# Kernel optimization log

Hardware: AMD Instinct MI355X
Metric: run time of the kernel (lower is better)

The kernel has to match this reference:

```python
import jax, jax.numpy as jnp
import numpy as np

T, B, H, L = 64, 128, 256, 2  # steps/stack_size, batch, hidden, layers


def setup_inputs() -> dict:
    key = jax.random.key(0)
    ks = jax.random.split(key, 6)
    s = 1.0 / np.sqrt(H)
    x = jax.random.normal(ks[0], (T, B, H), dtype=jnp.float32)
    ops = jax.random.randint(ks[1], (T, B), 0, 2, dtype=jnp.int32)  # push=1, hold=0
    W_ih = jax.random.uniform(ks[2], (L, 4 * H, H), jnp.float32, -s, s)
    W_hh = jax.random.uniform(ks[3], (L, 4 * H, H), jnp.float32, -s, s)
    b_ih = jax.random.uniform(ks[4], (L, 4 * H), jnp.float32, -s, s)
    b_hh = jax.random.uniform(ks[5], (L, 4 * H), jnp.float32, -s, s)
    return {"x": x, "ops": ops, "W_ih": W_ih, "W_hh": W_hh, "b_ih": b_ih, "b_hh": b_hh}


def reference(x, ops, W_ih, W_hh, b_ih, b_hh):
    T_, B_, H_ = x.shape
    L_ = W_ih.shape[0]
    bidx = jnp.arange(B_)

    def cell(xt, h_prev, c_prev):
        # multi-layer LSTM cell; layer l>0 takes layer l-1 hidden as input (dropout=0)
        inp = xt
        hs, cs = [], []
        for l in range(L_):
            gates = inp @ W_ih[l].T + b_ih[l] + h_prev[..., l] @ W_hh[l].T + b_hh[l]
            i, f, g, o = jnp.split(gates, 4, axis=-1)
            c = jax.nn.sigmoid(f) * c_prev[..., l] + jax.nn.sigmoid(i) * jnp.tanh(g)
            h = jax.nn.sigmoid(o) * jnp.tanh(c)
            hs.append(h)
            cs.append(c)
            inp = h
        return jnp.stack(hs, axis=-1), jnp.stack(cs, axis=-1)  # (B, H, L)

    def step(carry, xt_op):
        hstack, cstack, pos = carry  # stacks: (T+1, B, H, L), pos: (B,)
        xt, opt = xt_op
        h_prev = hstack[pos, bidx]  # gather top-of-stack, (B, H, L)
        c_prev = cstack[pos, bidx]
        nh, nc = cell(xt, h_prev, c_prev)
        # hold_or_push writes at pos+1 for every batch element, then pos += op
        hstack = hstack.at[pos + 1, bidx].set(nh)
        cstack = cstack.at[pos + 1, bidx].set(nc)
        pos = pos + opt
        return (hstack, cstack, pos), nh[..., -1]  # last-layer hidden output

    hs0 = jnp.zeros((T_ + 1, B_, H_, L_), dtype=x.dtype)
    cs0 = jnp.zeros((T_ + 1, B_, H_, L_), dtype=x.dtype)
    pos0 = jnp.zeros((B_,), dtype=jnp.int32)
    _, outs = jax.lax.scan(step, (hs0, cs0, pos0), (x, ops))
    return outs  # (T, B, H)
```

## Files before the change

kernel.cpp:

```cpp
#include <hip/hip_runtime.h>
#include <hip/hip_fp16.h>
#include <cstddef>

#define TT 64
#define BB 128
#define HH 256
#define G4 1024
#define BLK 256
#define NBG 32
#define NHG 16

#define OFF_XG     0u
#define OFF_WTIH0  8388608u
#define OFF_HX0    8650752u
#define OFF_HX1    8716288u

__device__ __forceinline__ float sigf(float x) { return 1.0f / (1.0f + expf(-x)); }

typedef _Float16 h2v __attribute__((ext_vector_type(2)));

__device__ __forceinline__ float dot2acc(unsigned w, unsigned h, float acc) {
#if __has_builtin(__builtin_amdgcn_fdot2)
  return __builtin_amdgcn_fdot2(__builtin_bit_cast(h2v, w),
                                __builtin_bit_cast(h2v, h), acc, false);
#else
  __half2 wv = *(__half2*)&w, hv = *(__half2*)&h;
  float2 wf = __half22float2(wv), hf = __half22float2(hv);
  return fmaf(wf.x, hf.x, fmaf(wf.y, hf.y, acc));
#endif
}

__device__ __forceinline__ unsigned packh2(float e, float o) {
  return (unsigned)__half_as_ushort(__float2half(e)) |
         ((unsigned)__half_as_ushort(__float2half(o)) << 16);
}

__device__ __forceinline__ int hsw(int b, int k2) {
  return b * 144 + k2 + ((k2 >> 5) << 2);
}

__global__ void transpose1(const float* __restrict__ W_ih, float* __restrict__ ws) {
  __shared__ float tile[32][33];
  float* dst = ws + OFF_WTIH0;
  const int g0 = blockIdx.x * 32, k0 = blockIdx.y * 32;
  const int tx = threadIdx.x, ty = threadIdx.y;
#pragma unroll
  for (int i = 0; i < 32; i += 8)
    tile[ty + i][tx] = W_ih[(size_t)(g0 + ty + i) * HH + k0 + tx];
  __syncthreads();
#pragma unroll
  for (int i = 0; i < 32; i += 8)
    dst[(size_t)(k0 + ty + i) * G4 + g0 + tx] = tile[tx][ty + i];
}

__global__ void xg_kernel(const float* __restrict__ x,
                          const float* __restrict__ b_ih,
                          float* __restrict__ ws) {
  const float* __restrict__ WTih0 = ws + OFF_WTIH0;
  float* __restrict__ Xg = ws + OFF_XG;
  const int r0 = blockIdx.x * 16;
  const int g = blockIdx.y * 256 + threadIdx.x;
  __shared__ float xs[16][HH];
  for (int i = threadIdx.x; i < 16 * HH; i += 256)
    xs[i >> 8][i & 255] = x[(size_t)(r0 + (i >> 8)) * HH + (i & 255)];
  __syncthreads();
  float acc[16];
  const float bias = b_ih[g];
#pragma unroll
  for (int r = 0; r < 16; ++r) acc[r] = bias;
  for (int k = 0; k < HH; ++k) {
    const float w = WTih0[(size_t)k * G4 + g];
#pragma unroll
    for (int r = 0; r < 16; ++r) acc[r] = fmaf(xs[r][k], w, acc[r]);
  }
  const int hg = (g >> 4) & 15;
  const int lc = ((g >> 8) << 4) | (g & 15);
#pragma unroll
  for (int r = 0; r < 16; ++r) {
    const int rr = r0 + r;
    const int t = rr >> 7, b = rr & 127;
    Xg[(((size_t)t * NHG + hg) * 128 + b) * 64 + lc] = acc[r];
  }
}

__global__ void __launch_bounds__(BLK, 2)
seq9(const float* __restrict__ W_ih,
     const float* __restrict__ W_hh,
     const float* __restrict__ b_ih,
     const float* __restrict__ b_hh,
     const int* __restrict__ ops,
     float* __restrict__ ws,
     float* __restrict__ out) {
  const int bg = blockIdx.x & 31;
  const int hg = blockIdx.x >> 5;
  const int tid = threadIdx.x;
  const int kq = tid & 7;
  const int c2 = tid >> 3;

  __shared__ __align__(16) float XgL[TT * 256];
  __shared__ __align__(16) unsigned hp0[4 * 144];
  __shared__ __align__(16) unsigned hp1[4 * 144];
  __shared__ __align__(16) unsigned h0c[4 * 144];
  __shared__ float gatA[256];
  __shared__ float gatB[256];
  __shared__ int opsA[TT * 4];

  unsigned wr0[32], wr1[32], wr2[32];
  {
    const float* s0 = W_hh;
    const float* s1 = W_ih + (size_t)G4 * HH;
    const float* s2 = W_hh + (size_t)G4 * HH;
#pragma unroll
    for (int j = 0; j < 2; ++j) {
      const int lc = c2 * 2 + j;
      const int g = ((lc >> 4) << 8) + hg * 16 + (lc & 15);
      const float* p0 = s0 + (size_t)g * HH + kq * 32;
      const float* p1 = s1 + (size_t)g * HH + kq * 32;
      const float* p2 = s2 + (size_t)g * HH + kq * 32;
#pragma unroll
      for (int i = 0; i < 16; ++i) {
        wr0[j * 16 + i] = packh2(p0[2 * i], p0[2 * i + 1]);
        wr1[j * 16 + i] = packh2(p1[2 * i], p1[2 * i + 1]);
        wr2[j * 16 + i] = packh2(p2[2 * i], p2[2 * i + 1]);
      }
    }
  }
  float bias0r[2], bias1r[2];
#pragma unroll
  for (int j = 0; j < 2; ++j) {
    const int lc = c2 * 2 + j;
    const int g = ((lc >> 4) << 8) + hg * 16 + (lc & 15);
    bias0r[j] = b_hh[g];
    bias1r[j] = b_ih[G4 + g] + b_hh[G4 + g];
  }
  for (int i = tid; i < TT * 64; i += BLK) {
    const int t = i >> 6, r = i & 63;
    ((float4*)XgL)[i] = *(const float4*)(
        ws + OFF_XG + (((size_t)t * NHG + hg) * 128 + bg * 4) * 64 + r * 4);
  }
  for (int i = tid; i < TT * 4; i += BLK)
    opsA[i] = ops[(i >> 2) * BB + bg * 4 + (i & 3)];
  for (int i = tid; i < 4 * 144; i += BLK) { hp0[i] = 0u; hp1[i] = 0u; }

  unsigned long long* __restrict__ Hx0 = (unsigned long long*)(ws + OFF_HX0);
  unsigned long long* __restrict__ Hx1 = (unsigned long long*)(ws + OFF_HX1);
  float cp0 = 0.f, cp1 = 0.f;
  float a0r[4][2] = {{0.f, 0.f}, {0.f, 0.f}, {0.f, 0.f}, {0.f, 0.f}};
  float a1q[4][2] = {{0.f, 0.f}, {0.f, 0.f}, {0.f, 0.f}, {0.f, 0.f}};
  __syncthreads();

  for (int t = 0; t < TT; ++t) {
    const int par = t & 1;

#pragma unroll
    for (int b = 0; b < 4; ++b) {
      if (t > 0 && opsA[(t - 1) * 4 + b]) {
        const unsigned* hb = &hp0[b * 144 + kq * 16 + ((kq >> 1) << 2)];
        const uint4 x0 = *(const uint4*)(hb + 0);
        const uint4 x1 = *(const uint4*)(hb + 4);
        const uint4 x2 = *(const uint4*)(hb + 8);
        const uint4 x3 = *(const uint4*)(hb + 12);
        const unsigned hh[16] = {x0.x, x0.y, x0.z, x0.w, x1.x, x1.y, x1.z, x1.w,
                                 x2.x, x2.y, x2.z, x2.w, x3.x, x3.y, x3.z, x3.w};
        float s0 = 0.f, s1 = 0.f;
#pragma unroll
        for (int i = 0; i < 16; ++i) {
          s0 = dot2acc(wr0[i], hh[i], s0);
          s1 = dot2acc(wr0[16 + i], hh[i], s1);
        }
#pragma unroll
        for (int m = 1; m <= 4; m <<= 1) {
          s0 += __shfl_xor(s0, m, 64);
          s1 += __shfl_xor(s1, m, 64);
        }
        a0r[b][0] = s0;
        a0r[b][1] = s1;
      }
    }
    if (kq == 0) {
#pragma unroll
      for (int b = 0; b < 4; ++b)
        *(float2*)&gatA[b * 64 + c2 * 2] =
            make_float2(a0r[b][0] + bias0r[0], a0r[b][1] + bias0r[1]);
    }
    __syncthreads();

    if (tid < 64) {
      const int b = tid >> 4, r = tid & 15;
      const float* xg = &XgL[t * 256 + b * 64];
      const float* gt = &gatA[b * 64];
      const float ig = gt[r] + xg[r],           fg = gt[16 + r] + xg[16 + r];
      const float gg = gt[32 + r] + xg[32 + r], og = gt[48 + r] + xg[48 + r];
      const float c = sigf(fg) * cp0 + sigf(ig) * tanhf(gg);
      const float h = sigf(og) * tanhf(c);
      if (opsA[t * 4 + b]) cp0 = c;
      const float ho = __shfl_xor(h, 1, 64);
      if (!(r & 1)) {
        const unsigned long long v =
            (unsigned long long)(unsigned)(t + 1) |
            ((unsigned long long)packh2(h, ho) << 32);
        __hip_atomic_store(
            Hx0 + ((size_t)par * NBG + bg) * 512 + b * 128 + hg * 8 + (r >> 1),
            v, __ATOMIC_RELAXED, __HIP_MEMORY_SCOPE_AGENT);
      }
    }

    {
      const unsigned long long* s0 = Hx0 + ((size_t)par * NBG + bg) * 512;
      const unsigned long long* s1 = Hx1 + ((size_t)(par ^ 1) * NBG + bg) * 512;
      const unsigned tagA = (unsigned)(t + 1);
      const unsigned tagB = (unsigned)t;
      const int idx1 = tid + 256;
      const int b0 = tid >> 7, k20 = tid & 127;
      const int b1 = idx1 >> 7, k21 = idx1 & 127;
      const bool need1a = (t > 0) && (opsA[(t - 1) * 4 + b0] != 0);
      const bool need1b = (t > 0) && (opsA[(t - 1) * 4 + b1] != 0);
      unsigned long long v0 = 0, v1 = 0, w0 = 0, w1 = 0;
      bool d0 = false, d1 = false, e0 = !need1a, e1 = !need1b;
      int spins = 0;
      for (;;) {
        if (!d0) v0 = __hip_atomic_load(s0 + tid, __ATOMIC_RELAXED,
                                        __HIP_MEMORY_SCOPE_AGENT);
        if (!d1) v1 = __hip_atomic_load(s0 + idx1, __ATOMIC_RELAXED,
                                        __HIP_MEMORY_SCOPE_AGENT);
        if (!e0) w0 = __hip_atomic_load(s1 + tid, __ATOMIC_RELAXED,
                                        __HIP_MEMORY_SCOPE_AGENT);
        if (!e1) w1 = __hip_atomic_load(s1 + idx1, __ATOMIC_RELAXED,
                                        __HIP_MEMORY_SCOPE_AGENT);
        d0 = d0 || ((unsigned)v0 == tagA);
        d1 = d1 || ((unsigned)v1 == tagA);
        e0 = e0 || ((unsigned)w0 == tagB);
        e1 = e1 || ((unsigned)w1 == tagB);
        if (d0 && d1 && e0 && e1) break;
        if (++spins > (1 << 18)) break;
        if (spins > 2) __builtin_amdgcn_s_sleep(1);
      }
      const unsigned p0 = (unsigned)(v0 >> 32), p1 = (unsigned)(v1 >> 32);
      const int sw0 = hsw(b0, k20), sw1 = hsw(b1, k21);
      h0c[sw0] = p0;
      h0c[sw1] = p1;
      if (opsA[t * 4 + b0]) hp0[sw0] = p0;
      if (opsA[t * 4 + b1]) hp0[sw1] = p1;
      if (need1a) hp1[sw0] = (unsigned)(w0 >> 32);
      if (need1b) hp1[sw1] = (unsigned)(w1 >> 32);
    }
    __syncthreads();

    float fr[4][2];
#pragma unroll
    for (int b = 0; b < 4; ++b) {
      const unsigned* cb = &h0c[b * 144 + kq * 16 + ((kq >> 1) << 2)];
      const uint4 c0 = *(const uint4*)(cb + 0);
      const uint4 c1 = *(const uint4*)(cb + 4);
      const uint4 c2v = *(const uint4*)(cb + 8);
      const uint4 c3 = *(const uint4*)(cb + 12);
      const unsigned hc[16] = {c0.x, c0.y, c0.z, c0.w, c1.x, c1.y, c1.z, c1.w,
                               c2v.x, c2v.y, c2v.z, c2v.w, c3.x, c3.y, c3.z, c3.w};
      float s0 = 0.f, s1 = 0.f;
#pragma unroll
      for (int i = 0; i < 16; ++i) {
        s0 = dot2acc(wr1[i], hc[i], s0);
        s1 = dot2acc(wr1[16 + i], hc[i], s1);
      }
      if (t > 0 && opsA[(t - 1) * 4 + b]) {
        const unsigned* qb = &hp1[b * 144 + kq * 16 + ((kq >> 1) << 2)];
        const uint4 q0 = *(const uint4*)(qb + 0);
        const uint4 q1 = *(const uint4*)(qb + 4);
        const uint4 q2 = *(const uint4*)(qb + 8);
        const uint4 q3 = *(const uint4*)(qb + 12);
        const unsigned hq[16] = {q0.x, q0.y, q0.z, q0.w, q1.x, q1.y, q1.z, q1.w,
                                 q2.x, q2.y, q2.z, q2.w, q3.x, q3.y, q3.z, q3.w};
        float t0 = 0.f, t1 = 0.f;
#pragma unroll
        for (int i = 0; i < 16; ++i) {
          t0 = dot2acc(wr2[i], hq[i], t0);
          t1 = dot2acc(wr2[16 + i], hq[i], t1);
        }
#pragma unroll
        for (int m = 1; m <= 4; m <<= 1) {
          t0 += __shfl_xor(t0, m, 64);
          t1 += __shfl_xor(t1, m, 64);
        }
        a1q[b][0] = t0;
        a1q[b][1] = t1;
      }
#pragma unroll
      for (int m = 1; m <= 4; m <<= 1) {
        s0 += __shfl_xor(s0, m, 64);
        s1 += __shfl_xor(s1, m, 64);
      }
      fr[b][0] = s0;
      fr[b][1] = s1;
    }
    if (kq == 0) {
#pragma unroll
      for (int b = 0; b < 4; ++b)
        *(float2*)&gatB[b * 64 + c2 * 2] =
            make_float2(fr[b][0] + a1q[b][0] + bias1r[0],
                        fr[b][1] + a1q[b][1] + bias1r[1]);
    }
    __syncthreads();

    if (tid < 64) {
      const int b = tid >> 4, r = tid & 15;
      const float* gt = &gatB[b * 64];
      const float ig = gt[r],      fg = gt[16 + r];
      const float gg = gt[32 + r], og = gt[48 + r];
      const float c = sigf(fg) * cp1 + sigf(ig) * tanhf(gg);
      const float h = sigf(og) * tanhf(c);
      const int op = opsA[t * 4 + b];
      if (op) cp1 = c;
      out[((size_t)t * BB + bg * 4 + b) * HH + hg * 16 + r] = h;
      const float ho = __shfl_xor(h, 1, 64);
      if (op && !(r & 1)) {
        const unsigned long long v =
            (unsigned long long)(unsigned)(t + 1) |
            ((unsigned long long)packh2(h, ho) << 32);
        __hip_atomic_store(
            Hx1 + ((size_t)par * NBG + bg) * 512 + b * 128 + hg * 8 + (r >> 1),
            v, __ATOMIC_RELAXED, __HIP_MEMORY_SCOPE_AGENT);
      }
    }
  }
}

extern "C" void kernel_launch(void* const* d_in, const int* in_sizes, int n_in,
                              void* d_out, int out_size, void* d_ws, size_t ws_size,
                              hipStream_t stream) {
  const float* x    = (const float*)d_in[0];
  const int*   ops  = (const int*)d_in[1];
  const float* W_ih = (const float*)d_in[2];
  const float* W_hh = (const float*)d_in[3];
  const float* b_ih = (const float*)d_in[4];
  const float* b_hh = (const float*)d_in[5];
  float* out = (float*)d_out;
  float* ws  = (float*)d_ws;

  transpose1<<<dim3(32, 8), dim3(32, 8), 0, stream>>>(W_ih, ws);
  xg_kernel<<<dim3(512, 4), 256, 0, stream>>>(x, b_ih, ws);
  seq9<<<512, BLK, 0, stream>>>(W_ih, W_hh, b_ih, b_hh, ops, ws, out);
}
```

Before: 523.9 us.

## Split layers into separate pipelined block roles and fuse input projection

Replaces the three-kernel pipeline with one persistent kernel whose blocks take one of two roles: layer-0 blocks and layer-1 blocks, each handling 8 batch rows per block. Layer 0 now computes the x·W_ih projection in-kernel with double-buffered x loads, which removes the separate transpose and precompute kernels and their workspace traffic. Layer-1 blocks consume layer-0 hidden states through per-timestep tagged global buffers, so the two layers can run in a wavefront pipeline instead of serially within a block. The cost is more register pressure (64 fp32 weights per thread in layer 0), larger global handoff buffers, and cross-block spin waiting.

New measurement: 467.1 us. -10.8%, faster.

```diff
diff --git a/kernel.cpp b/kernel.cpp
--- a/kernel.cpp
+++ b/kernel.cpp
@@ -7,13 +7,8 @@
 #define HH 256
 #define G4 1024
 #define BLK 256
-#define NBG 32
+#define NBG 16
 #define NHG 16
-
-#define OFF_XG     0u
-#define OFF_WTIH0  8388608u
-#define OFF_HX0    8650752u
-#define OFF_HX1    8716288u
 
 __device__ __forceinline__ float sigf(float x) { return 1.0f / (1.0f + expf(-x)); }
 
@@ -35,290 +30,333 @@
          ((unsigned)__half_as_ushort(__float2half(o)) << 16);
 }
 
-__device__ __forceinline__ int hsw(int b, int k2) {
+__device__ __forceinline__ int hsw8(int b, int k2) {
   return b * 144 + k2 + ((k2 >> 5) << 2);
 }
 
-__global__ void transpose1(const float* __restrict__ W_ih, float* __restrict__ ws) {
-  __shared__ float tile[32][33];
-  float* dst = ws + OFF_WTIH0;
-  const int g0 = blockIdx.x * 32, k0 = blockIdx.y * 32;
-  const int tx = threadIdx.x, ty = threadIdx.y;
-#pragma unroll
-  for (int i = 0; i < 32; i += 8)
-    tile[ty + i][tx] = W_ih[(size_t)(g0 + ty + i) * HH + k0 + tx];
-  __syncthreads();
-#pragma unroll
-  for (int i = 0; i < 32; i += 8)
-    dst[(size_t)(k0 + ty + i) * G4 + g0 + tx] = tile[tx][ty + i];
-}
-
-__global__ void xg_kernel(const float* __restrict__ x,
-                          const float* __restrict__ b_ih,
-                          float* __restrict__ ws) {
-  const float* __restrict__ WTih0 = ws + OFF_WTIH0;
-  float* __restrict__ Xg = ws + OFF_XG;
-  const int r0 = blockIdx.x * 16;
-  const int g = blockIdx.y * 256 + threadIdx.x;
-  __shared__ float xs[16][HH];
-  for (int i = threadIdx.x; i < 16 * HH; i += 256)
-    xs[i >> 8][i & 255] = x[(size_t)(r0 + (i >> 8)) * HH + (i & 255)];
-  __syncthreads();
-  float acc[16];
-  const float bias = b_ih[g];
-#pragma unroll
-  for (int r = 0; r < 16; ++r) acc[r] = bias;
-  for (int k = 0; k < HH; ++k) {
-    const float w = WTih0[(size_t)k * G4 + g];
-#pragma unroll
-    for (int r = 0; r < 16; ++r) acc[r] = fmaf(xs[r][k], w, acc[r]);
-  }
-  const int hg = (g >> 4) & 15;
-  const int lc = ((g >> 8) << 4) | (g & 15);
-#pragma unroll
-  for (int r = 0; r < 16; ++r) {
-    const int rr = r0 + r;
-    const int t = rr >> 7, b = rr & 127;
-    Xg[(((size_t)t * NHG + hg) * 128 + b) * 64 + lc] = acc[r];
-  }
-}
-
 __global__ void __launch_bounds__(BLK, 2)
-seq9(const float* __restrict__ W_ih,
-     const float* __restrict__ W_hh,
-     const float* __restrict__ b_ih,
-     const float* __restrict__ b_hh,
-     const int* __restrict__ ops,
-     float* __restrict__ ws,
-     float* __restrict__ out) {
-  const int bg = blockIdx.x & 31;
-  const int hg = blockIdx.x >> 5;
+seq10(const float* __restrict__ x,
+      const int* __restrict__ ops,
+      const float* __restrict__ W_ih,
+      const float* __restrict__ W_hh,
+      const float* __restrict__ b_ih,
+      const float* __restrict__ b_hh,
+      float* __restrict__ ws,
+      float* __restrict__ out) {
+  const int role = blockIdx.x >> 8;
+  const int bh = blockIdx.x & 255;
+  const int bg = bh & 15;
+  const int hg = bh >> 4;
   const int tid = threadIdx.x;
   const int kq = tid & 7;
   const int c2 = tid >> 3;
 
-  __shared__ __align__(16) float XgL[TT * 256];
-  __shared__ __align__(16) unsigned hp0[4 * 144];
-  __shared__ __align__(16) unsigned hp1[4 * 144];
-  __shared__ __align__(16) unsigned h0c[4 * 144];
-  __shared__ float gatA[256];
-  __shared__ float gatB[256];
-  __shared__ int opsA[TT * 4];
-
-  unsigned wr0[32], wr1[32], wr2[32];
-  {
-    const float* s0 = W_hh;
-    const float* s1 = W_ih + (size_t)G4 * HH;
-    const float* s2 = W_hh + (size_t)G4 * HH;
+  __shared__ __align__(16) float smem[6272];
+  __shared__ int opsA[TT * 8];
+
+  unsigned long long* __restrict__ Hx0 = (unsigned long long*)ws;
+  unsigned long long* __restrict__ Hx1 = Hx0 + (size_t)TT * NBG * 1024;
+
+  for (int i = tid; i < TT * 8; i += BLK)
+    opsA[i] = ops[(i >> 3) * BB + bg * 8 + (i & 7)];
+
+  const int pb = tid >> 5;
+  const int pk2 = (tid & 31) * 4;
+
+  if (role == 0) {
+    float* xbufs = smem;
+    unsigned* hp0 = (unsigned*)(smem + 4608);
+    float* gatA = smem + 5760;
+
+    unsigned wr0[32];
+    float wx0[64];
+    float bias0r[2];
 #pragma unroll
     for (int j = 0; j < 2; ++j) {
       const int lc = c2 * 2 + j;
       const int g = ((lc >> 4) << 8) + hg * 16 + (lc & 15);
-      const float* p0 = s0 + (size_t)g * HH + kq * 32;
-      const float* p1 = s1 + (size_t)g * HH + kq * 32;
-      const float* p2 = s2 + (size_t)g * HH + kq * 32;
+      const float* ph = W_hh + (size_t)g * HH + kq * 32;
+      const float* pw = W_ih + (size_t)g * HH + kq * 32;
+#pragma unroll
+      for (int i = 0; i < 16; ++i)
+        wr0[j * 16 + i] = packh2(ph[2 * i], ph[2 * i + 1]);
+#pragma unroll
+      for (int i = 0; i < 32; ++i) wx0[j * 32 + i] = pw[i];
+      bias0r[j] = b_ih[g] + b_hh[g];
+    }
+    for (int i = tid; i < 8 * 144; i += BLK) hp0[i] = 0u;
+    {
+      const float4* xsrc = (const float4*)(x + (size_t)bg * 8 * HH);
+#pragma unroll
+      for (int i2 = 0; i2 < 2; ++i2) {
+        const int f4 = tid + i2 * 256;
+        const float4 v = xsrc[f4];
+        const int b = f4 >> 6, k4 = f4 & 63;
+        *(float4*)&xbufs[b * 288 + (k4 >> 3) * 36 + (k4 & 7) * 4] = v;
+      }
+    }
+    __syncthreads();
+
+    float xf[8][2];
+#pragma unroll
+    for (int b = 0; b < 8; ++b) {
+      const float* xb = &xbufs[b * 288 + kq * 36];
+      float s0 = 0.f, s1 = 0.f;
+#pragma unroll
+      for (int k = 0; k < 32; ++k) {
+        s0 = fmaf(wx0[k], xb[k], s0);
+        s1 = fmaf(wx0[32 + k], xb[k], s1);
+      }
+#pragma unroll
+      for (int m = 1; m <= 4; m <<= 1) {
+        s0 += __shfl_xor(s0, m, 64);
+        s1 += __shfl_xor(s1, m, 64);
+      }
+      xf[b][0] = s0; xf[b][1] = s1;
+    }
+    float a0r[8][2] = {};
+    float cp0 = 0.f;
+
+    for (int t = 0; t < TT; ++t) {
+      if (t > 0 && opsA[(t - 1) * 8 + pb]) {
+        const unsigned long long* sp = Hx0 + ((size_t)(t - 1) * NBG + bg) * 1024;
+        const unsigned tag = (unsigned)t;
+        unsigned long long v[4];
+        bool d[4] = {false, false, false, false};
+        int spins = 0;
+        for (;;) {
+#pragma unroll
+          for (int i = 0; i < 4; ++i)
+            if (!d[i]) v[i] = __hip_atomic_load(sp + tid * 4 + i, __ATOMIC_RELAXED,
+                                                __HIP_MEMORY_SCOPE_AGENT);
+          bool all = true;
+#pragma unroll
+          for (int i = 0; i < 4; ++i) { d[i] = d[i] || ((unsigned)v[i] == tag); all &= d[i]; }
+          if (all) break;
+          if (++spins > (1 << 18)) break;
+          if (spins > 2) __builtin_amdgcn_s_sleep(1);
+        }
+        *(uint4*)&hp0[hsw8(pb, pk2)] =
+            make_uint4((unsigned)(v[0] >> 32), (unsigned)(v[1] >> 32),
+                       (unsigned)(v[2] >> 32), (unsigned)(v[3] >> 32));
+      }
+      __syncthreads();
+
+#pragma unroll
+      for (int b = 0; b < 8; ++b) {
+        if (t > 0 && opsA[(t - 1) * 8 + b]) {
+          const unsigned* hb = &hp0[b * 144 + kq * 16 + ((kq >> 1) << 2)];
+          const uint4 x0 = *(const uint4*)(hb + 0);
+          const uint4 x1 = *(const uint4*)(hb + 4);
+          const uint4 x2 = *(const uint4*)(hb + 8);
+          const uint4 x3 = *(const uint4*)(hb + 12);
+          const unsigned hh[16] = {x0.x, x0.y, x0.z, x0.w, x1.x, x1.y, x1.z, x1.w,
+                                   x2.x, x2.y, x2.z, x2.w, x3.x, x3.y, x3.z, x3.w};
+          float s0 = 0.f, s1 = 0.f;
+#pragma unroll
+          for (int i = 0; i < 16; ++i) {
+            s0 = dot2acc(wr0[i], hh[i], s0);
+            s1 = dot2acc(wr0[16 + i], hh[i], s1);
+          }
+#pragma unroll
+          for (int m = 1; m <= 4; m <<= 1) {
+            s0 += __shfl_xor(s0, m, 64);
+            s1 += __shfl_xor(s1, m, 64);
+          }
+          a0r[b][0] = s0; a0r[b][1] = s1;
+        }
+      }
+      if (kq == 0) {
+#pragma unroll
+        for (int b = 0; b < 8; ++b)
+          *(float2*)&gatA[b * 64 + c2 * 2] =
+              make_float2(xf[b][0] + a0r[b][0] + bias0r[0],
+                          xf[b][1] + a0r[b][1] + bias0r[1]);
+      }
+      __syncthreads();
+
+      if (tid < 128) {
+        const int b = tid >> 4, r = tid & 15;
+        const float* gt = &gatA[b * 64];
+        const float ig = gt[r], fg = gt[16 + r], gg = gt[32 + r], og = gt[48 + r];
+        const float c = sigf(fg) * cp0 + sigf(ig) * tanhf(gg);
+        const float h = sigf(og) * tanhf(c);
+        if (opsA[t * 8 + b]) cp0 = c;
+        const float ho = __shfl_xor(h, 1, 64);
+        if (!(r & 1)) {
+          const unsigned long long vv =
+              (unsigned long long)(unsigned)(t + 1) |
+              ((unsigned long long)packh2(h, ho) << 32);
+          __hip_atomic_store(
+              Hx0 + ((size_t)t * NBG + bg) * 1024 + b * 128 + hg * 8 + (r >> 1),
+              vv, __ATOMIC_RELAXED, __HIP_MEMORY_SCOPE_AGENT);
+        }
+      }
+      if (t < TT - 1) {
+        float* xd = &xbufs[((t + 1) & 1) * 2304];
+        const float4* xsrc = (const float4*)(x + ((size_t)(t + 1) * BB + bg * 8) * HH);
+#pragma unroll
+        for (int i2 = 0; i2 < 2; ++i2) {
+          const int f4 = tid + i2 * 256;
+          const float4 v = xsrc[f4];
+          const int b = f4 >> 6, k4 = f4 & 63;
+          *(float4*)&xd[b * 288 + (k4 >> 3) * 36 + (k4 & 7) * 4] = v;
+        }
+        __syncthreads();
+#pragma unroll
+        for (int b = 0; b < 8; ++b) {
+          const float* xb = &xd[b * 288 + kq * 36];
+          float s0 = 0.f, s1 = 0.f;
+#pragma unroll
+          for (int k = 0; k < 32; ++k) {
+            s0 = fmaf(wx0[k], xb[k], s0);
+            s1 = fmaf(wx0[32 + k], xb[k], s1);
+          }
+#pragma unroll
+          for (int m = 1; m <= 4; m <<= 1) {
+            s0 += __shfl_xor(s0, m, 64);
+            s1 += __shfl_xor(s1, m, 64);
+          }
+          xf[b][0] = s0; xf[b][1] = s1;
+        }
+      }
+    }
+  } else {
+    unsigned* h0c = (unsigned*)smem;
+    unsigned* hp1 = (unsigned*)(smem + 1152);
+    float* gatB = smem + 2304;
+
+    unsigned wr1[32], wr2[32];
+    float bias1r[2];
+#pragma unroll
+    for (int j = 0; j < 2; ++j) {
+      const int lc = c2 * 2 + j;
+      const int g = ((lc >> 4) << 8) + hg * 16 + (lc & 15);
+      const float* p1 = W_ih + (size_t)G4 * HH + (size_t)g * HH + kq * 32;
+      const float* p2 = W_hh + (size_t)G4 * HH + (size_t)g * HH + kq * 32;
 #pragma unroll
       for (int i = 0; i < 16; ++i) {
-        wr0[j * 16 + i] = packh2(p0[2 * i], p0[2 * i + 1]);
         wr1[j * 16 + i] = packh2(p1[2 * i], p1[2 * i + 1]);
         wr2[j * 16 + i] = packh2(p2[2 * i], p2[2 * i + 1]);
       }
-    }
-  }
-  float bias0r[2], bias1r[2];
-#pragma unroll
-  for (int j = 0; j < 2; ++j) {
-    const int lc = c2 * 2 + j;
-    const int g = ((lc >> 4) << 8) + hg * 16 + (lc & 15);
-    bias0r[j] = b_hh[g];
-    bias1r[j] = b_ih[G4 + g] + b_hh[G4 + g];
-  }
-  for (int i = tid; i < TT * 64; i += BLK) {
-    const int t = i >> 6, r = i & 63;
-    ((float4*)XgL)[i] = *(const float4*)(
-        ws + OFF_XG + (((size_t)t * NHG + hg) * 128 + bg * 4) * 64 + r * 4);
-  }
-  for (int i = tid; i < TT * 4; i += BLK)
-    opsA[i] = ops[(i >> 2) * BB + bg * 4 + (i & 3)];
-  for (int i = tid; i < 4 * 144; i += BLK) { hp0[i] = 0u; hp1[i] = 0u; }
-
-  unsigned long long* __restrict__ Hx0 = (unsigned long long*)(ws + OFF_HX0);
-  unsigned long long* __restrict__ Hx1 = (unsigned long long*)(ws + OFF_HX1);
-  float cp0 = 0.f, cp1 = 0.f;
-  float a0r[4][2] = {{0.f, 0.f}, {0.f, 0.f}, {0.f, 0.f}, {0.f, 0.f}};
-  float a1q[4][2] = {{0.f, 0.f}, {0.f, 0.f}, {0.f, 0.f}, {0.f, 0.f}};
-  __syncthreads();
-
-  for (int t = 0; t < TT; ++t) {
-    const int par = t & 1;
-
-#pragma unroll
-    for (int b = 0; b < 4; ++b) {
-      if (t > 0 && opsA[(t - 1) * 4 + b]) {
-        const unsigned* hb = &hp0[b * 144 + kq * 16 + ((kq >> 1) << 2)];
-        const uint4 x0 = *(const uint4*)(hb + 0);
-        const uint4 x1 = *(const uint4*)(hb + 4);
-        const uint4 x2 = *(const uint4*)(hb + 8);
-        const uint4 x3 = *(const uint4*)(hb + 12);
-        const unsigned hh[16] = {x0.x, x0.y, x0.z, x0.w, x1.x, x1.y, x1.z, x1.w,
-                                 x2.x, x2.y, x2.z, x2.w, x3.x, x3.y, x3.z, x3.w};
+      bias1r[j] = b_ih[G4 + g] + b_hh[G4 + g];
+    }
+    for (int i = tid; i < 8 * 144; i += BLK) hp1[i] = 0u;
+    float a1q[8][2] = {};
+    float cp1 = 0.f;
+    __syncthreads();
+
+    for (int t = 0; t < TT; ++t) {
+      {
+        const unsigned long long* sp0 = Hx0 + ((size_t)t * NBG + bg) * 1024;
+        const unsigned long long* sp1 =
+            Hx1 + ((size_t)(t > 0 ? t - 1 : 0) * NBG + bg) * 1024;
+        const unsigned tagA = (unsigned)(t + 1), tagB = (unsigned)t;
+        const bool need1 = (t > 0) && (opsA[(t - 1) * 8 + pb] != 0);
+        unsigned long long v[4], w[4];
+        bool dv[4] = {false, false, false, false};
+        bool dw[4] = {!need1, !need1, !need1, !need1};
+        int spins = 0;
+        for (;;) {
+#pragma unroll
+          for (int i = 0; i < 4; ++i) {
+            if (!dv[i]) v[i] = __hip_atomic_load(sp0 + tid * 4 + i, __ATOMIC_RELAXED,
+                                                 __HIP_MEMORY_SCOPE_AGENT);
+            if (!dw[i]) w[i] = __hip_atomic_load(sp1 + tid * 4 + i, __ATOMIC_RELAXED,
+                                                 __HIP_MEMORY_SCOPE_AGENT);
+          }
+          bool all = true;
+#pragma unroll
+          for (int i = 0; i < 4; ++i) {
+            dv[i] = dv[i] || ((unsigned)v[i] == tagA);
+            dw[i] = dw[i] || ((unsigned)w[i] == tagB);
+            all = all && dv[i] && dw[i];
+          }
+          if (all) break;
+          if (++spins > (1 << 18)) break;
+          if (spins > 2) __builtin_amdgcn_s_sleep(1);
+        }
+        *(uint4*)&h0c[hsw8(pb, pk2)] =
+            make_uint4((unsigned)(v[0] >> 32), (unsigned)(v[1] >> 32),
+                       (unsigned)(v[2] >> 32), (unsigned)(v[3] >> 32));
+        if (need1)
+          *(uint4*)&hp1[hsw8(pb, pk2)] =
+              make_uint4((unsigned)(w[0] >> 32), (unsigned)(w[1] >> 32),
+                         (unsigned)(w[2] >> 32), (unsigned)(w[3] >> 32));
+      }
+      __syncthreads();
+
+      float fr[8][2];
+#pragma unroll
+      for (int b = 0; b < 8; ++b) {
+        const unsigned* cb = &h0c[b * 144 + kq * 16 + ((kq >> 1) << 2)];
+        const uint4 c0 = *(const uint4*)(cb + 0);
+        const uint4 c1 = *(const uint4*)(cb + 4);
+        const uint4 c2v = *(const uint4*)(cb + 8);
+        const uint4 c3 = *(const uint4*)(cb + 12);
+        const unsigned hc[16] = {c0.x, c0.y, c0.z, c0.w, c1.x, c1.y, c1.z, c1.w,
+                                 c2v.x, c2v.y, c2v.z, c2v.w, c3.x, c3.y, c3.z, c3.w};
         float s0 = 0.f, s1 = 0.f;
 #pragma unroll
         for (int i = 0; i < 16; ++i) {
-          s0 = dot2acc(wr0[i], hh[i], s0);
-          s1 = dot2acc(wr0[16 + i], hh[i], s1);
+          s0 = dot2acc(wr1[i], hc[i], s0);
+          s1 = dot2acc(wr1[16 + i], hc[i], s1);
+        }
+        if (t > 0 && opsA[(t - 1) * 8 + b]) {
+          const unsigned* qb = &hp1[b * 144 + kq * 16 + ((kq >> 1) << 2)];
+          const uint4 q0 = *(const uint4*)(qb + 0);
+          const uint4 q1 = *(const uint4*)(qb + 4);
+          const uint4 q2 = *(const uint4*)(qb + 8);
+          const uint4 q3 = *(const uint4*)(qb + 12);
+          const unsigned hq[16] = {q0.x, q0.y, q0.z, q0.w, q1.x, q1.y, q1.z, q1.w,
+                                   q2.x, q2.y, q2.z, q2.w, q3.x, q3.y, q3.z, q3.w};
+          float t0 = 0.f, t1 = 0.f;
+#pragma unroll
+          for (int i = 0; i < 16; ++i) {
+            t0 = dot2acc(wr2[i], hq[i], t0);
+            t1 = dot2acc(wr2[16 + i], hq[i], t1);
+          }
+#pragma unroll
+          for (int m = 1; m <= 4; m <<= 1) {
+            t0 += __shfl_xor(t0, m, 64);
+            t1 += __shfl_xor(t1, m, 64);
+          }
+          a1q[b][0] = t0; a1q[b][1] = t1;
         }
 #pragma unroll
         for (int m = 1; m <= 4; m <<= 1) {
           s0 += __shfl_xor(s0, m, 64);
           s1 += __shfl_xor(s1, m, 64);
         }
-        a0r[b][0] = s0;
-        a0r[b][1] = s1;
-      }
-    }
-    if (kq == 0) {
-#pragma unroll
-      for (int b = 0; b < 4; ++b)
-        *(float2*)&gatA[b * 64 + c2 * 2] =
-            make_float2(a0r[b][0] + bias0r[0], a0r[b][1] + bias0r[1]);
-    }
-    __syncthreads();
-
-    if (tid < 64) {
-      const int b = tid >> 4, r = tid & 15;
-      const float* xg = &XgL[t * 256 + b * 64];
-      const float* gt = &gatA[b * 64];
-      const float ig = gt[r] + xg[r],           fg = gt[16 + r] + xg[16 + r];
-      const float gg = gt[32 + r] + xg[32 + r], og = gt[48 + r] + xg[48 + r];
-      const float c = sigf(fg) * cp0 + sigf(ig) * tanhf(gg);
-      const float h = sigf(og) * tanhf(c);
-      if (opsA[t * 4 + b]) cp0 = c;
-      const float ho = __shfl_xor(h, 1, 64);
-      if (!(r & 1)) {
-        const unsigned long long v =
-            (unsigned long long)(unsigned)(t + 1) |
-            ((unsigned long long)packh2(h, ho) << 32);
-        __hip_atomic_store(
-            Hx0 + ((size_t)par * NBG + bg) * 512 + b * 128 + hg * 8 + (r >> 1),
-            v, __ATOMIC_RELAXED, __HIP_MEMORY_SCOPE_AGENT);
-      }
-    }
-
-    {
-      const unsigned long long* s0 = Hx0 + ((size_t)par * NBG + bg) * 512;
-      const unsigned long long* s1 = Hx1 + ((size_t)(par ^ 1) * NBG + bg) * 512;
-      const unsigned tagA = (unsigned)(t + 1);
-      const unsigned tagB = (unsigned)t;
-      const int idx1 = tid + 256;
-      const int b0 = tid >> 7, k20 = tid & 127;
-      const int b1 = idx1 >> 7, k21 = idx1 & 127;
-      const bool need1a = (t > 0) && (opsA[(t - 1) * 4 + b0] != 0);
-      const bool need1b = (t > 0) && (opsA[(t - 1) * 4 + b1] != 0);
-      unsigned long long v0 = 0, v1 = 0, w0 = 0, w1 = 0;
-      bool d0 = false, d1 = false, e0 = !need1a, e1 = !need1b;
-      int spins = 0;
-      for (;;) {
-        if (!d0) v0 = __hip_atomic_load(s0 + tid, __ATOMIC_RELAXED,
-                                        __HIP_MEMORY_SCOPE_AGENT);
-        if (!d1) v1 = __hip_atomic_load(s0 + idx1, __ATOMIC_RELAXED,
-                                        __HIP_MEMORY_SCOPE_AGENT);
-        if (!e0) w0 = __hip_atomic_load(s1 + tid, __ATOMIC_RELAXED,
-                                        __HIP_MEMORY_SCOPE_AGENT);
-        if (!e1) w1 = __hip_atomic_load(s1 + idx1, __ATOMIC_RELAXED,
-                                        __HIP_MEMORY_SCOPE_AGENT);
-        d0 = d0 || ((unsigned)v0 == tagA);
-        d1 = d1 || ((unsigned)v1 == tagA);
-        e0 = e0 || ((unsigned)w0 == tagB);
-        e1 = e1 || ((unsigned)w1 == tagB);
-        if (d0 && d1 && e0 && e1) break;
-        if (++spins > (1 << 18)) break;
-        if (spins > 2) __builtin_amdgcn_s_sleep(1);
-      }
-      const unsigned p0 = (unsigned)(v0 >> 32), p1 = (unsigned)(v1 >> 32);
-      const int sw0 = hsw(b0, k20), sw1 = hsw(b1, k21);
-      h0c[sw0] = p0;
-      h0c[sw1] = p1;
-      if (opsA[t * 4 + b0]) hp0[sw0] = p0;
-      if (opsA[t * 4 + b1]) hp0[sw1] = p1;
-      if (need1a) hp1[sw0] = (unsigned)(w0 >> 32);
-      if (need1b) hp1[sw1] = (unsigned)(w1 >> 32);
-    }
-    __syncthreads();
-
-    float fr[4][2];
-#pragma unroll
-    for (int b = 0; b < 4; ++b) {
-      const unsigned* cb = &h0c[b * 144 + kq * 16 + ((kq >> 1) << 2)];
-      const uint4 c0 = *(const uint4*)(cb + 0);
-      const uint4 c1 = *(const uint4*)(cb + 4);
-      const uint4 c2v = *(const uint4*)(cb + 8);
-      const uint4 c3 = *(const uint4*)(cb + 12);
-      const unsigned hc[16] = {c0.x, c0.y, c0.z, c0.w, c1.x, c1.y, c1.z, c1.w,
-                               c2v.x, c2v.y, c2v.z, c2v.w, c3.x, c3.y, c3.z, c3.w};
-      float s0 = 0.f, s1 = 0.f;
-#pragma unroll
-      for (int i = 0; i < 16; ++i) {
-        s0 = dot2acc(wr1[i], hc[i], s0);
-        s1 = dot2acc(wr1[16 + i], hc[i], s1);
-      }
-      if (t > 0 && opsA[(t - 1) * 4 + b]) {
-        const unsigned* qb = &hp1[b * 144 + kq * 16 + ((kq >> 1) << 2)];
-        const uint4 q0 = *(const uint4*)(qb + 0);
-        const uint4 q1 = *(const uint4*)(qb + 4);
-        const uint4 q2 = *(const uint4*)(qb + 8);
-        const uint4 q3 = *(const uint4*)(qb + 12);
-        const unsigned hq[16] = {q0.x, q0.y, q0.z, q0.w, q1.x, q1.y, q1.z, q1.w,
-                                 q2.x, q2.y, q2.z, q2.w, q3.x, q3.y, q3.z, q3.w};
-        float t0 = 0.f, t1 = 0.f;
-#pragma unroll
-        for (int i = 0; i < 16; ++i) {
-          t0 = dot2acc(wr2[i], hq[i], t0);
-          t1 = dot2acc(wr2[16 + i], hq[i], t1);
-        }
-#pragma unroll
-        for (int m = 1; m <= 4; m <<= 1) {
-          t0 += __shfl_xor(t0, m, 64);
-          t1 += __shfl_xor(t1, m, 64);
-        }
-        a1q[b][0] = t0;
-        a1q[b][1] = t1;
-      }
-#pragma unroll
-      for (int m = 1; m <= 4; m <<= 1) {
-        s0 += __shfl_xor(s0, m, 64);
-        s1 += __shfl_xor(s1, m, 64);
-      }
-      fr[b][0] = s0;
-      fr[b][1] = s1;
-    }
-    if (kq == 0) {
-#pragma unroll
-      for (int b = 0; b < 4; ++b)
-        *(float2*)&gatB[b * 64 + c2 * 2] =
-            make_float2(fr[b][0] + a1q[b][0] + bias1r[0],
-                        fr[b][1] + a1q[b][1] + bias1r[1]);
-    }
-    __syncthreads();
-
-    if (tid < 64) {
-      const int b = tid >> 4, r = tid & 15;
-      const float* gt = &gatB[b * 64];
-      const float ig = gt[r],      fg = gt[16 + r];
-      const float gg = gt[32 + r], og = gt[48 + r];
-      const float c = sigf(fg) * cp1 + sigf(ig) * tanhf(gg);
-      const float h = sigf(og) * tanhf(c);
-      const int op = opsA[t * 4 + b];
-      if (op) cp1 = c;
-      out[((size_t)t * BB + bg * 4 + b) * HH + hg * 16 + r] = h;
-      const float ho = __shfl_xor(h, 1, 64);
-      if (op && !(r & 1)) {
-        const unsigned long long v =
-            (unsigned long long)(unsigned)(t + 1) |
-            ((unsigned long long)packh2(h, ho) << 32);
-        __hip_atomic_store(
-            Hx1 + ((size_t)par * NBG + bg) * 512 + b * 128 + hg * 8 + (r >> 1),
-            v, __ATOMIC_RELAXED, __HIP_MEMORY_SCOPE_AGENT);
+        fr[b][0] = s0; fr[b][1] = s1;
+      }
+      if (kq == 0) {
+#pragma unroll
+        for (int b = 0; b < 8; ++b)
+          *(float2*)&gatB[b * 64 + c2 * 2] =
+              make_float2(fr[b][0] + a1q[b][0] + bias1r[0],
+                          fr[b][1] + a1q[b][1] + bias1r[1]);
+      }
+      __syncthreads();
+
+      if (tid < 128) {
+        const int b = tid >> 4, r = tid & 15;
+        const float* gt = &gatB[b * 64];
+        const float ig = gt[r], fg = gt[16 + r], gg = gt[32 + r], og = gt[48 + r];
+        const float c = sigf(fg) * cp1 + sigf(ig) * tanhf(gg);
+        const float h = sigf(og) * tanhf(c);
+        const int op = opsA[t * 8 + b];
+        if (op) cp1 = c;
+        out[((size_t)t * BB + bg * 8 + b) * HH + hg * 16 + r] = h;
+        const float ho = __shfl_xor(h, 1, 64);
+        if (op && !(r & 1)) {
+          const unsigned long long vv =
+              (unsigned long long)(unsigned)(t + 1) |
+              ((unsigned long long)packh2(h, ho) << 32);
+          __hip_atomic_store(
+              Hx1 + ((size_t)t * NBG + bg) * 1024 + b * 128 + hg * 8 + (r >> 1),
+              vv, __ATOMIC_RELAXED, __HIP_MEMORY_SCOPE_AGENT);
+        }
       }
     }
   }
@@ -336,7 +374,5 @@
   float* out = (float*)d_out;
   float* ws  = (float*)d_ws;
 
-  transpose1<<<dim3(32, 8), dim3(32, 8), 0, stream>>>(W_ih, ws);
-  xg_kernel<<<dim3(512, 4), 256, 0, stream>>>(x, b_ih, ws);
-  seq9<<<512, BLK, 0, stream>>>(W_ih, W_hh, b_ih, b_hh, ops, ws, out);
-}
+  seq10<<<512, BLK, 0, stream>>>(x, ops, W_ih, W_hh, b_ih, b_hh, ws, out);
+}
```

## Fuse layer-0 input projection into the sequential LSTM kernel prologue

Applied to the files above, without the earlier changes.

Removes the separate weight-transpose and input-projection kernels. Each block of the persistent recurrent kernel now computes its own slice of the x·W_ih0 gate preactivations, using fp32 weights held in registers and shuffle reductions, and writes them straight into shared memory. This saves two kernel launches and the global round trip of the 8M-float Xg buffer. In exchange the prologue runs serially inside the recurrent kernel, keeps 64 extra registers live for a while, and each block reads x for its batch rows across all 64 steps.

Result: slower. 870.7 us (+66.2%).

```diff
diff --git a/kernel.cpp b/kernel.cpp
--- a/kernel.cpp
+++ b/kernel.cpp
@@ -8,12 +8,9 @@
 #define G4 1024
 #define BLK 256
 #define NBG 32
-#define NHG 16
-
-#define OFF_XG     0u
-#define OFF_WTIH0  8388608u
-#define OFF_HX0    8650752u
-#define OFF_HX1    8716288u
+
+#define OFF_HX0 0u
+#define OFF_HX1 65536u
 
 __device__ __forceinline__ float sigf(float x) { return 1.0f / (1.0f + expf(-x)); }
 
@@ -39,58 +36,15 @@
   return b * 144 + k2 + ((k2 >> 5) << 2);
 }
 
-__global__ void transpose1(const float* __restrict__ W_ih, float* __restrict__ ws) {
-  __shared__ float tile[32][33];
-  float* dst = ws + OFF_WTIH0;
-  const int g0 = blockIdx.x * 32, k0 = blockIdx.y * 32;
-  const int tx = threadIdx.x, ty = threadIdx.y;
-#pragma unroll
-  for (int i = 0; i < 32; i += 8)
-    tile[ty + i][tx] = W_ih[(size_t)(g0 + ty + i) * HH + k0 + tx];
-  __syncthreads();
-#pragma unroll
-  for (int i = 0; i < 32; i += 8)
-    dst[(size_t)(k0 + ty + i) * G4 + g0 + tx] = tile[tx][ty + i];
-}
-
-__global__ void xg_kernel(const float* __restrict__ x,
-                          const float* __restrict__ b_ih,
-                          float* __restrict__ ws) {
-  const float* __restrict__ WTih0 = ws + OFF_WTIH0;
-  float* __restrict__ Xg = ws + OFF_XG;
-  const int r0 = blockIdx.x * 16;
-  const int g = blockIdx.y * 256 + threadIdx.x;
-  __shared__ float xs[16][HH];
-  for (int i = threadIdx.x; i < 16 * HH; i += 256)
-    xs[i >> 8][i & 255] = x[(size_t)(r0 + (i >> 8)) * HH + (i & 255)];
-  __syncthreads();
-  float acc[16];
-  const float bias = b_ih[g];
-#pragma unroll
-  for (int r = 0; r < 16; ++r) acc[r] = bias;
-  for (int k = 0; k < HH; ++k) {
-    const float w = WTih0[(size_t)k * G4 + g];
-#pragma unroll
-    for (int r = 0; r < 16; ++r) acc[r] = fmaf(xs[r][k], w, acc[r]);
-  }
-  const int hg = (g >> 4) & 15;
-  const int lc = ((g >> 8) << 4) | (g & 15);
-#pragma unroll
-  for (int r = 0; r < 16; ++r) {
-    const int rr = r0 + r;
-    const int t = rr >> 7, b = rr & 127;
-    Xg[(((size_t)t * NHG + hg) * 128 + b) * 64 + lc] = acc[r];
-  }
-}
-
 __global__ void __launch_bounds__(BLK, 2)
-seq9(const float* __restrict__ W_ih,
-     const float* __restrict__ W_hh,
-     const float* __restrict__ b_ih,
-     const float* __restrict__ b_hh,
-     const int* __restrict__ ops,
-     float* __restrict__ ws,
-     float* __restrict__ out) {
+seq12(const float* __restrict__ x,
+      const int* __restrict__ ops,
+      const float* __restrict__ W_ih,
+      const float* __restrict__ W_hh,
+      const float* __restrict__ b_ih,
+      const float* __restrict__ b_hh,
+      float* __restrict__ ws,
+      float* __restrict__ out) {
   const int bg = blockIdx.x & 31;
   const int hg = blockIdx.x >> 5;
   const int tid = threadIdx.x;
@@ -105,6 +59,50 @@
   __shared__ float gatB[256];
   __shared__ int opsA[TT * 4];
 
+  for (int i = tid; i < TT * 4; i += BLK)
+    opsA[i] = ops[(i >> 2) * BB + bg * 4 + (i & 3)];
+  for (int i = tid; i < 4 * 144; i += BLK) { hp0[i] = 0u; hp1[i] = 0u; }
+
+  {
+    float wx0[64], pb0[2];
+#pragma unroll
+    for (int j = 0; j < 2; ++j) {
+      const int lc = c2 * 2 + j;
+      const int g = ((lc >> 4) << 8) + hg * 16 + (lc & 15);
+      const float* pw = W_ih + (size_t)g * HH + kq * 32;
+#pragma unroll
+      for (int i = 0; i < 32; ++i) wx0[j * 32 + i] = pw[i];
+      pb0[j] = b_ih[g];
+    }
+    for (int t = 0; t < TT; ++t) {
+#pragma unroll
+      for (int b = 0; b < 4; ++b) {
+        const float* xp = x + ((size_t)t * BB + bg * 4 + b) * HH + kq * 32;
+        float s0 = 0.f, s1 = 0.f;
+#pragma unroll
+        for (int k = 0; k < 32; k += 4) {
+          const float4 xv = *(const float4*)(xp + k);
+          s0 = fmaf(wx0[k], xv.x, s0);
+          s0 = fmaf(wx0[k + 1], xv.y, s0);
+          s0 = fmaf(wx0[k + 2], xv.z, s0);
+          s0 = fmaf(wx0[k + 3], xv.w, s0);
+          s1 = fmaf(wx0[32 + k], xv.x, s1);
+          s1 = fmaf(wx0[32 + k + 1], xv.y, s1);
+          s1 = fmaf(wx0[32 + k + 2], xv.z, s1);
+          s1 = fmaf(wx0[32 + k + 3], xv.w, s1);
+        }
+#pragma unroll
+        for (int m = 1; m <= 4; m <<= 1) {
+          s0 += __shfl_xor(s0, m, 64);
+          s1 += __shfl_xor(s1, m, 64);
+        }
+        if (kq == 0)
+          *(float2*)&XgL[t * 256 + b * 64 + c2 * 2] =
+              make_float2(s0 + pb0[0], s1 + pb0[1]);
+      }
+    }
+  }
+
   unsigned wr0[32], wr1[32], wr2[32];
   {
     const float* s0 = W_hh;
@@ -133,14 +131,6 @@
     bias0r[j] = b_hh[g];
     bias1r[j] = b_ih[G4 + g] + b_hh[G4 + g];
   }
-  for (int i = tid; i < TT * 64; i += BLK) {
-    const int t = i >> 6, r = i & 63;
-    ((float4*)XgL)[i] = *(const float4*)(
-        ws + OFF_XG + (((size_t)t * NHG + hg) * 128 + bg * 4) * 64 + r * 4);
-  }
-  for (int i = tid; i < TT * 4; i += BLK)
-    opsA[i] = ops[(i >> 2) * BB + bg * 4 + (i & 3)];
-  for (int i = tid; i < 4 * 144; i += BLK) { hp0[i] = 0u; hp1[i] = 0u; }
 
   unsigned long long* __restrict__ Hx0 = (unsigned long long*)(ws + OFF_HX0);
   unsigned long long* __restrict__ Hx1 = (unsigned long long*)(ws + OFF_HX1);
@@ -336,7 +326,5 @@
   float* out = (float*)d_out;
   float* ws  = (float*)d_ws;
 
-  transpose1<<<dim3(32, 8), dim3(32, 8), 0, stream>>>(W_ih, ws);
-  xg_kernel<<<dim3(512, 4), 256, 0, stream>>>(x, b_ih, ws);
-  seq9<<<512, BLK, 0, stream>>>(W_ih, W_hh, b_ih, b_hh, ops, ws, out);
-}
+  seq12<<<512, BLK, 0, stream>>>(x, ops, W_ih, W_hh, b_ih, b_hh, ws, out);
+}
```
